# Kernel optimization log

Hardware: AMD Instinct MI355X
Metric: run time of the kernel (lower is better)

Reference implementation:

```python
import jax, jax.numpy as jnp
import numpy as np

B, S, DM = 2, 2048, 2048
H, KV, HD = 16, 4, 128
THETA = 10000.0
EPS = 1e-6


def _rmsnorm(x, scale):
    # flax nnx.RMSNorm with dtype=float32: x / sqrt(mean(x^2)+eps) * scale
    var = jnp.mean(jnp.square(x.astype(jnp.float32)), axis=-1, keepdims=True)
    return (x.astype(jnp.float32) * jax.lax.rsqrt(var + EPS)) * scale


def _apply_rope(x, positions, base):
    # x: [B, S, heads, HD]; positions: [1, S]
    half = HD // 2
    fraction = 2.0 * jnp.arange(half, dtype=jnp.float32) / HD
    timescale = base ** fraction                              # [HD/2]
    sinusoid = positions[..., None].astype(jnp.float32) / timescale  # [1, S, HD/2]
    sinusoid = sinusoid[..., None, :]                         # [1, S, 1, HD/2]
    sin, cos = jnp.sin(sinusoid), jnp.cos(sinusoid)
    x1, x2 = x[..., :half], x[..., half:]
    return jnp.concatenate([x1 * cos - x2 * sin, x2 * cos + x1 * sin], axis=-1).astype(x.dtype)


def setup_inputs() -> dict:
    key = jax.random.key(0)
    ks = jax.random.split(key, 7)
    w = lambda k, shape: jax.random.normal(k, shape, jnp.float32) * 0.02
    return {
        "x": jax.random.normal(ks[0], (B, S, DM), jnp.float32),
        "wq": w(ks[1], (DM, H, HD)),
        "wk": w(ks[2], (DM, KV, HD)),
        "wv": w(ks[3], (DM, KV, HD)),
        "wo": w(ks[4], (H, HD, DM)),
        "q_scale": jnp.ones((HD,), jnp.float32),
        "k_scale": jnp.ones((HD,), jnp.float32),
    }


def reference(x, wq, wk, wv, wo, q_scale, k_scale):
    # QKV projections (LinearGeneral hidden -> (heads, head_dim))
    q = jnp.einsum("bsd,dhk->bshk", x, wq)   # [B,S,H,HD]
    k = jnp.einsum("bsd,dhk->bshk", x, wk)   # [B,S,KV,HD]
    v = jnp.einsum("bsd,dhk->bshk", x, wv)   # [B,S,KV,HD]
    # qk RMSNorm + cast back to compute dtype
    q = _rmsnorm(q, q_scale).astype(x.dtype)
    k = _rmsnorm(k, k_scale).astype(x.dtype)
    # RoPE
    positions = jnp.arange(S)[None, :]
    q = _apply_rope(q, positions, THETA)
    k = _apply_rope(k, positions, THETA)
    # GQA attention: group query heads per kv head instead of materializing repeat_kv
    G = H // KV
    qg = q.reshape(B, S, KV, G, HD) * (HD ** -0.5)
    scores = jnp.einsum("bqkgd,bskd->bkgqs", qg, k)           # [B,KV,G,S,S]
    causal = jnp.tril(jnp.ones((S, S), jnp.bool_))
    scores = jnp.where(causal, scores, jnp.finfo(scores.dtype).min)
    probs = jax.nn.softmax(scores, axis=-1)
    att = jnp.einsum("bkgqs,bskd->bqkgd", probs, v).reshape(B, S, H, HD)
    # output projection contracting (heads, head_dim)
    return jnp.einsum("bshd,hdo->bso", att, wo)
```

## Files before the change

kernel.cpp:

```cpp
#include <hip/hip_runtime.h>
#include <hip/hip_bf16.h>
#include <math.h>

typedef unsigned short u16;
typedef short short8 __attribute__((ext_vector_type(8)));
typedef float floatx4 __attribute__((ext_vector_type(4)));

#define B_   2
#define S_   2048
#define DM_  2048
#define H_   16
#define KVH_ 4
#define HD_  128

__device__ __forceinline__ float bf2f(u16 v) {
  union { unsigned int u; float f; } x; x.u = ((unsigned int)v) << 16; return x.f;
}
__device__ __forceinline__ u16 f2bf(float f) {
  union { float f; unsigned int u; } x; x.f = f;
  unsigned int u = x.u;
  u += 0x7FFFu + ((u >> 16) & 1u);
  return (u16)(u >> 16);
}

#define GLDS16(gp, lp) __builtin_amdgcn_global_load_lds( \
    (const __attribute__((address_space(1))) unsigned int*)(const void*)(gp), \
    (__attribute__((address_space(3))) unsigned int*)(void*)(lp), 16, 0, 0)

__global__ __launch_bounds__(256) void k_prep(
    const float* __restrict__ x, const float* __restrict__ wq,
    const float* __restrict__ wk, const float* __restrict__ wv,
    const float* __restrict__ wo,
    u16* __restrict__ x_bf, u16* __restrict__ wqkv_t, u16* __restrict__ wo_t)
{
  int bx = blockIdx.x;
  if (bx < 8192) {
    int i = bx * 256 + threadIdx.x;
    const float4 v = ((const float4*)x)[i];
    u16 o[4] = { f2bf(v.x), f2bf(v.y), f2bf(v.z), f2bf(v.w) };
    *(unsigned long long*)(x_bf + (size_t)i * 4) = *(unsigned long long*)o;
    return;
  }
  bx -= 8192;
  const float* src; u16* dst; int C, cb;
  if (bx < 4096)      { src = wq; dst = wqkv_t; C = 2048; cb = 64; }
  else if (bx < 5120) { bx -= 4096; src = wk; dst = wqkv_t + (size_t)2048 * 2048; C = 512; cb = 16; }
  else if (bx < 6144) { bx -= 5120; src = wv; dst = wqkv_t + (size_t)2560 * 2048; C = 512; cb = 16; }
  else                { bx -= 6144; src = wo; dst = wo_t; C = 2048; cb = 64; }
  const int R = 2048;
  int c0 = (bx % cb) * 32, r0 = (bx / cb) * 32;
  __shared__ float tile[32][33];
  int tx = threadIdx.x & 31, ty = threadIdx.x >> 5;
#pragma unroll
  for (int j = 0; j < 4; j++)
    tile[ty * 4 + j][tx] = src[(size_t)(r0 + ty * 4 + j) * C + c0 + tx];
  __syncthreads();
#pragma unroll
  for (int j = 0; j < 4; j++)
    dst[(size_t)(c0 + ty * 4 + j) * R + r0 + tx] = f2bf(tile[tx][ty * 4 + j]);
}

__global__ __launch_bounds__(256, 3) void k_gemm_bt(
    const u16* __restrict__ A, const u16* __restrict__ Bt,
    void* __restrict__ Cout, int M, int N, int K, int c_bf16)
{
  __shared__ u16 As[128 * 64];
  __shared__ u16 Bs[128 * 64];
  int tid = threadIdx.x;
  int lane = tid & 63;
  int quad = lane >> 4, l16 = lane & 15;
  int wid = tid >> 6;
  int m0 = blockIdx.y * 128, n0 = blockIdx.x * 128;
  int wm = (wid >> 1) * 64, wn = (wid & 1) * 64;

  floatx4 acc[4][4] = {};

  int srow = tid >> 3;
  int gjc0 = (tid & 7) ^ (srow & 7);
  const u16* Ap = A + (size_t)(m0 + srow) * K + gjc0 * 8;
  const u16* Bp = Bt + (size_t)(n0 + srow) * K + gjc0 * 8;
  u16* AsW = As + tid * 8;
  u16* BsW = Bs + tid * 8;

  for (int kt = 0; kt < K; kt += 64) {
    __syncthreads();
#pragma unroll
    for (int j = 0; j < 4; j++) {
      GLDS16(Ap + (size_t)(j * 32) * K, AsW + j * 2048);
      GLDS16(Bp + (size_t)(j * 32) * K, BsW + j * 2048);
    }
    Ap += 64; Bp += 64;
    __syncthreads();

#pragma unroll
    for (int ks = 0; ks < 2; ks++) {
      short8 af[4], bfv[4];
#pragma unroll
      for (int mi = 0; mi < 4; mi++) {
        int row = wm + mi * 16 + l16;
        af[mi] = *(const short8*)&As[row * 64 + (((ks * 4 + quad) ^ (row & 7)) * 8)];
      }
#pragma unroll
      for (int ni = 0; ni < 4; ni++) {
        int row = wn + ni * 16 + l16;
        bfv[ni] = *(const short8*)&Bs[row * 64 + (((ks * 4 + quad) ^ (row & 7)) * 8)];
      }
#pragma unroll
      for (int mi = 0; mi < 4; mi++)
#pragma unroll
        for (int ni = 0; ni < 4; ni++)
          acc[mi][ni] = __builtin_amdgcn_mfma_f32_16x16x32_bf16(
              af[mi], bfv[ni], acc[mi][ni], 0, 0, 0);
    }
  }

#pragma unroll
  for (int mi = 0; mi < 4; mi++)
#pragma unroll
    for (int ni = 0; ni < 4; ni++)
#pragma unroll
      for (int r = 0; r < 4; r++) {
        int row = m0 + wm + mi * 16 + quad * 4 + r;
        int col = n0 + wn + ni * 16 + l16;
        float v = acc[mi][ni][r];
        if (c_bf16) ((u16*)Cout)[(size_t)row * N + col] = f2bf(v);
        else        ((float*)Cout)[(size_t)row * N + col] = v;
      }
}

__global__ __launch_bounds__(256) void k_post(
    const u16* __restrict__ C1, const float* __restrict__ qs,
    const float* __restrict__ ks, u16* __restrict__ qr, u16* __restrict__ kr,
    u16* __restrict__ vt)
{
  int bx = blockIdx.x;
  if (bx < 4096) {
    int m = bx;
    int lane = threadIdx.x & 63, wid = threadIdx.x >> 6;
    int pos = m & (S_ - 1);
    float ts = powf(10000.0f, (float)lane * (1.0f / 64.0f));
    float ang = (float)pos / ts;
    float sn = sinf(ang), cs = cosf(ang);
    for (int r = wid; r < H_ + KVH_; r += 4) {
      bool isq = r < H_;
      const u16* src = C1 + (size_t)m * 3072 + (isq ? r * HD_ : DM_ + (r - H_) * HD_);
      float x1 = bf2f(src[lane]), x2 = bf2f(src[lane + 64]);
      float ss = x1 * x1 + x2 * x2;
#pragma unroll
      for (int d = 1; d < 64; d <<= 1) ss += __shfl_xor(ss, d);
      float rs = rsqrtf(ss * (1.0f / 128.0f) + 1e-6f);
      const float* sc = isq ? qs : ks;
      float y1 = x1 * rs * sc[lane];
      float y2 = x2 * rs * sc[lane + 64];
      float o1 = y1 * cs - y2 * sn;
      float o2 = y2 * cs + y1 * sn;
      if (isq) { o1 *= 0.088388347648318447f; o2 *= 0.088388347648318447f; }
      u16* dst = isq ? (qr + ((size_t)m * H_ + r) * HD_)
                     : (kr + ((size_t)m * KVH_ + (r - H_)) * HD_);
      dst[lane]      = f2bf(o1);
      dst[lane + 64] = f2bf(o2);
    }
    return;
  }
  bx -= 4096;
  int sx = bx & 63, rest = bx >> 6;
  int hy = rest & 3, bk = rest >> 2;
  int s0 = sx * 32, h0 = hy * 32;
  int b = bk >> 2, kv = bk & 3;
  __shared__ u16 tile[32][33];
  int tx = threadIdx.x & 31, ty = threadIdx.x >> 5;
#pragma unroll
  for (int j = 0; j < 4; j++)
    tile[ty * 4 + j][tx] =
        C1[(size_t)(b * S_ + s0 + ty * 4 + j) * 3072 + 2560 + kv * HD_ + h0 + tx];
  __syncthreads();
#pragma unroll
  for (int j = 0; j < 4; j++)
    vt[((size_t)bk * HD_ + h0 + ty * 4 + j) * S_ + s0 + tx] = tile[tx][ty * 4 + j];
}

__global__ __launch_bounds__(256, 3) void k_flash(
    const u16* __restrict__ qr, const u16* __restrict__ kr,
    const u16* __restrict__ vt, u16* __restrict__ att)
{
  __shared__ u16 Ks[64 * 128];
  __shared__ u16 Vt[128 * 64];
  __shared__ u16 Ps[4][16 * 72];
  int tid = threadIdx.x, lane = tid & 63, wid = tid >> 6;
  int quad = lane >> 4, l16 = lane & 15;
  int bx = blockIdx.x;
  int it = 31 - (bx >> 5);
  int hb = bx & 31;
  int h = hb & 15, b = hb >> 4;
  int kvh = h >> 2;
  int q0 = it * 64;

  short8 qf[4];
  {
    const u16* qb = qr + ((size_t)(b * S_ + q0 + wid * 16 + l16) * H_ + h) * HD_;
#pragma unroll
    for (int kk = 0; kk < 4; kk++)
      qf[kk] = *(const short8*)(qb + kk * 32 + quad * 8);
  }

  int gjk = (tid & 15) ^ ((tid >> 4) & 15);
  int gjv = (tid & 7) ^ ((tid >> 3) & 7);
  const u16* kp = kr + ((size_t)(b * S_ + (tid >> 4)) * KVH_ + kvh) * HD_ + gjk * 8;
  const u16* vp = vt + ((size_t)(b * KVH_ + kvh) * HD_ + (tid >> 3)) * S_ + gjv * 8;

  short8 pk[4], pv[4];
#pragma unroll
  for (int j = 0; j < 4; j++) {
    pk[j] = *(const short8*)(kp + (size_t)j * 16 * KVH_ * HD_);
    pv[j] = *(const short8*)(vp + (size_t)j * 32 * S_);
  }

  floatx4 accO[8] = {};
  float lp[4] = { 0.f, 0.f, 0.f, 0.f };
  u16* PsW = &Ps[wid][0];
  int qrow_hi = q0 + wid * 16 + quad * 4;

  const float LOG2E = 1.4426950408889634f;
  const float MBIAS = -12.5f * 1.4426950408889634f;

  for (int kt = 0; kt <= it; kt++) {
    int k0 = kt * 64;
#pragma unroll
    for (int j = 0; j < 4; j++) {
      *(short8*)&Ks[(j * 256 + tid) * 8] = pk[j];
      *(short8*)&Vt[(j * 256 + tid) * 8] = pv[j];
    }
    __syncthreads();

    if (kt < it) {
      kp += (size_t)64 * KVH_ * HD_;
      vp += 64;
#pragma unroll
      for (int j = 0; j < 4; j++) {
        pk[j] = *(const short8*)(kp + (size_t)j * 16 * KVH_ * HD_);
        pv[j] = *(const short8*)(vp + (size_t)j * 32 * S_);
      }
    }

    floatx4 sacc[4] = {};
#pragma unroll
    for (int kk = 0; kk < 4; kk++)
#pragma unroll
      for (int nt = 0; nt < 4; nt++) {
        int row = nt * 16 + l16;
        short8 kf = *(const short8*)&Ks[row * 128 + (((kk * 4 + quad) ^ (row & 15)) * 8)];
        sacc[nt] = __builtin_amdgcn_mfma_f32_16x16x32_bf16(qf[kk], kf, sacc[nt], 0, 0, 0);
      }

    bool diag = (kt == it);
#pragma unroll
    for (int r = 0; r < 4; r++) {
      int row = qrow_hi + r;
      float rsum = 0.f;
#pragma unroll
      for (int nt = 0; nt < 4; nt++) {
        float p = __builtin_amdgcn_exp2f(fmaf(sacc[nt][r], LOG2E, MBIAS));
        if (diag && (k0 + nt * 16 + l16) > row) p = 0.f;
        rsum += p;
        PsW[(quad * 4 + r) * 72 + nt * 16 + l16] = f2bf(p);
      }
      lp[r] += rsum;
    }

#pragma unroll
    for (int kk = 0; kk < 2; kk++) {
      short8 pf = *(const short8*)&PsW[l16 * 72 + kk * 32 + quad * 8];
#pragma unroll
      for (int ht = 0; ht < 8; ht++) {
        int row = ht * 16 + l16;
        short8 vf = *(const short8*)&Vt[row * 64 + (((kk * 4 + quad) ^ (row & 7)) * 8)];
        accO[ht] = __builtin_amdgcn_mfma_f32_16x16x32_bf16(pf, vf, accO[ht], 0, 0, 0);
      }
    }
    __syncthreads();
  }

#pragma unroll
  for (int r = 0; r < 4; r++) {
#pragma unroll
    for (int d = 1; d < 16; d <<= 1) lp[r] += __shfl_xor(lp[r], d);
    lp[r] = 1.0f / lp[r];
  }

#pragma unroll
  for (int ht = 0; ht < 8; ht++)
#pragma unroll
    for (int r = 0; r < 4; r++) {
      int row = qrow_hi + r;
      att[((size_t)(b * S_ + row) * H_ + h) * HD_ + ht * 16 + l16] = f2bf(accO[ht][r] * lp[r]);
    }
}

extern "C" void kernel_launch(void* const* d_in, const int* in_sizes, int n_in,
                              void* d_out, int out_size, void* d_ws, size_t ws_size,
                              hipStream_t stream)
{
  const float* x  = (const float*)d_in[0];
  const float* wq = (const float*)d_in[1];
  const float* wk = (const float*)d_in[2];
  const float* wv = (const float*)d_in[3];
  const float* wo = (const float*)d_in[4];
  const float* qs = (const float*)d_in[5];
  const float* ks = (const float*)d_in[6];

  char* ws = (char*)d_ws;
  size_t off = 0;
  u16* x_bf   = (u16*)(ws + off); off += (size_t)4096 * 2048 * 2;
  u16* wqkv_t = (u16*)(ws + off); off += (size_t)3072 * 2048 * 2;
  u16* wo_t   = (u16*)(ws + off); off += (size_t)2048 * 2048 * 2;
  u16* C1     = (u16*)(ws + off); off += (size_t)4096 * 3072 * 2;
  u16* q_rope = (u16*)(ws + off); off += (size_t)4096 * 16 * 128 * 2;
  u16* k_rope = (u16*)(ws + off); off += (size_t)4096 * 4 * 128 * 2;
  u16* vt     = (u16*)(ws + off); off += (size_t)8 * 128 * 2048 * 2;
  u16* att    = (u16*)(ws + off); off += (size_t)4096 * 2048 * 2;

  k_prep<<<dim3(18432), 256, 0, stream>>>(x, wq, wk, wv, wo, x_bf, wqkv_t, wo_t);

  k_gemm_bt<<<dim3(24, 32), 256, 0, stream>>>(x_bf, wqkv_t, C1, 4096, 3072, 2048, 1);

  k_post<<<dim3(6144), 256, 0, stream>>>(C1, qs, ks, q_rope, k_rope, vt);

  k_flash<<<dim3(1024), 256, 0, stream>>>(q_rope, k_rope, vt, att);

  k_gemm_bt<<<dim3(16, 32), 256, 0, stream>>>(att, wo_t, d_out, 4096, 2048, 2048, 0);

  (void)in_sizes; (void)n_in; (void)out_size; (void)ws_size;
}
```

Measured before the change: 297.6 us.

## Restructure flash attention to 2 waves each owning 32 query rows

The flash attention kernel now runs 128 threads (2 waves) per block instead of 256 (4 waves). Each wave handles two 16-row query tiles, so every K and V fragment read from LDS feeds two MFMAs. The P buffer gets an XOR-swizzled layout, and s_setprio is raised around the MFMA sections. The intent is to cut LDS traffic per MFMA and raise compute density. The cost is higher register pressure, more global loads per thread for staging, and fewer waves per block to hide latency.

```diff
diff --git a/kernel.cpp b/kernel.cpp
--- a/kernel.cpp
+++ b/kernel.cpp
@@ -179,13 +179,13 @@
     vt[((size_t)bk * HD_ + h0 + ty * 4 + j) * S_ + s0 + tx] = tile[tx][ty * 4 + j];
 }
 
-__global__ __launch_bounds__(256, 3) void k_flash(
+__global__ __launch_bounds__(128, 2) void k_flash(
     const u16* __restrict__ qr, const u16* __restrict__ kr,
     const u16* __restrict__ vt, u16* __restrict__ att)
 {
   __shared__ u16 Ks[64 * 128];
   __shared__ u16 Vt[128 * 64];
-  __shared__ u16 Ps[4][16 * 72];
+  __shared__ u16 Ps[2][32 * 64];
   int tid = threadIdx.x, lane = tid & 63, wid = tid >> 6;
   int quad = lane >> 4, l16 = lane & 15;
   int bx = blockIdx.x;
@@ -195,30 +195,30 @@
   int kvh = h >> 2;
   int q0 = it * 64;
 
-  short8 qf[4];
-  {
-    const u16* qb = qr + ((size_t)(b * S_ + q0 + wid * 16 + l16) * H_ + h) * HD_;
+  short8 qf[2][4];
+#pragma unroll
+  for (int m = 0; m < 2; m++) {
+    const u16* qb = qr + ((size_t)(b * S_ + q0 + wid * 32 + m * 16 + l16) * H_ + h) * HD_;
 #pragma unroll
     for (int kk = 0; kk < 4; kk++)
-      qf[kk] = *(const short8*)(qb + kk * 32 + quad * 8);
-  }
-
-  int gjk = (tid & 15) ^ ((tid >> 4) & 15);
-  int gjv = (tid & 7) ^ ((tid >> 3) & 7);
-  const u16* kp = kr + ((size_t)(b * S_ + (tid >> 4)) * KVH_ + kvh) * HD_ + gjk * 8;
-  const u16* vp = vt + ((size_t)(b * KVH_ + kvh) * HD_ + (tid >> 3)) * S_ + gjv * 8;
-
-  short8 pk[4], pv[4];
-#pragma unroll
-  for (int j = 0; j < 4; j++) {
-    pk[j] = *(const short8*)(kp + (size_t)j * 16 * KVH_ * HD_);
-    pv[j] = *(const short8*)(vp + (size_t)j * 32 * S_);
-  }
-
-  floatx4 accO[8] = {};
-  float lp[4] = { 0.f, 0.f, 0.f, 0.f };
+      qf[m][kk] = *(const short8*)(qb + kk * 32 + quad * 8);
+  }
+
+  int gK = (tid & 15) ^ (tid >> 4);
+  int gV = (tid & 7) ^ ((tid >> 3) & 7);
+  const u16* kp = kr + ((size_t)(b * S_ + (tid >> 4)) * KVH_ + kvh) * HD_;
+  const u16* vp = vt + ((size_t)(b * KVH_ + kvh) * HD_ + (tid >> 3)) * S_ + gV * 8;
+
+  short8 pk[8], pv[8];
+#pragma unroll
+  for (int j = 0; j < 8; j++) {
+    pk[j] = *(const short8*)(kp + (size_t)(j * 8) * KVH_ * HD_ + (gK ^ ((j & 1) << 3)) * 8);
+    pv[j] = *(const short8*)(vp + (size_t)(j * 16) * S_);
+  }
+
+  floatx4 accO[2][8] = {};
+  float lp[2][4] = {};
   u16* PsW = &Ps[wid][0];
-  int qrow_hi = q0 + wid * 16 + quad * 4;
 
   const float LOG2E = 1.4426950408889634f;
   const float MBIAS = -12.5f * 1.4426950408889634f;
@@ -226,9 +226,9 @@
   for (int kt = 0; kt <= it; kt++) {
     int k0 = kt * 64;
 #pragma unroll
-    for (int j = 0; j < 4; j++) {
-      *(short8*)&Ks[(j * 256 + tid) * 8] = pk[j];
-      *(short8*)&Vt[(j * 256 + tid) * 8] = pv[j];
+    for (int j = 0; j < 8; j++) {
+      *(short8*)&Ks[(j * 128 + tid) * 8] = pk[j];
+      *(short8*)&Vt[(j * 128 + tid) * 8] = pv[j];
     }
     __syncthreads();
 
@@ -236,64 +236,88 @@
       kp += (size_t)64 * KVH_ * HD_;
       vp += 64;
 #pragma unroll
-      for (int j = 0; j < 4; j++) {
-        pk[j] = *(const short8*)(kp + (size_t)j * 16 * KVH_ * HD_);
-        pv[j] = *(const short8*)(vp + (size_t)j * 32 * S_);
-      }
-    }
-
-    floatx4 sacc[4] = {};
-#pragma unroll
-    for (int kk = 0; kk < 4; kk++)
+      for (int j = 0; j < 8; j++) {
+        pk[j] = *(const short8*)(kp + (size_t)(j * 8) * KVH_ * HD_ + (gK ^ ((j & 1) << 3)) * 8);
+        pv[j] = *(const short8*)(vp + (size_t)(j * 16) * S_);
+      }
+    }
+
+    floatx4 sacc[2][4] = {};
+    __builtin_amdgcn_s_setprio(1);
+#pragma unroll
+    for (int kk = 0; kk < 4; kk++) {
+      short8 kf[4];
 #pragma unroll
       for (int nt = 0; nt < 4; nt++) {
         int row = nt * 16 + l16;
-        short8 kf = *(const short8*)&Ks[row * 128 + (((kk * 4 + quad) ^ (row & 15)) * 8)];
-        sacc[nt] = __builtin_amdgcn_mfma_f32_16x16x32_bf16(qf[kk], kf, sacc[nt], 0, 0, 0);
-      }
+        kf[nt] = *(const short8*)&Ks[row * 128 + (((kk * 4 + quad) ^ (row & 15)) * 8)];
+      }
+#pragma unroll
+      for (int nt = 0; nt < 4; nt++) {
+        sacc[0][nt] = __builtin_amdgcn_mfma_f32_16x16x32_bf16(qf[0][kk], kf[nt], sacc[0][nt], 0, 0, 0);
+        sacc[1][nt] = __builtin_amdgcn_mfma_f32_16x16x32_bf16(qf[1][kk], kf[nt], sacc[1][nt], 0, 0, 0);
+      }
+    }
+    __builtin_amdgcn_s_setprio(0);
 
     bool diag = (kt == it);
 #pragma unroll
-    for (int r = 0; r < 4; r++) {
-      int row = qrow_hi + r;
-      float rsum = 0.f;
-#pragma unroll
-      for (int nt = 0; nt < 4; nt++) {
-        float p = __builtin_amdgcn_exp2f(fmaf(sacc[nt][r], LOG2E, MBIAS));
-        if (diag && (k0 + nt * 16 + l16) > row) p = 0.f;
-        rsum += p;
-        PsW[(quad * 4 + r) * 72 + nt * 16 + l16] = f2bf(p);
-      }
-      lp[r] += rsum;
-    }
-
+    for (int m = 0; m < 2; m++)
+#pragma unroll
+      for (int r = 0; r < 4; r++) {
+        int prow = m * 16 + quad * 4 + r;
+        int qrow = q0 + wid * 32 + prow;
+        float rsum = 0.f;
+#pragma unroll
+        for (int nt = 0; nt < 4; nt++) {
+          float p = __builtin_amdgcn_exp2f(fmaf(sacc[m][nt][r], LOG2E, MBIAS));
+          if (diag && (k0 + nt * 16 + l16) > qrow) p = 0.f;
+          rsum += p;
+          PsW[prow * 64 + (((nt * 2 + (l16 >> 3)) ^ (prow & 7)) * 8) + (l16 & 7)] = f2bf(p);
+        }
+        lp[m][r] += rsum;
+      }
+
+    __builtin_amdgcn_s_setprio(1);
 #pragma unroll
     for (int kk = 0; kk < 2; kk++) {
-      short8 pf = *(const short8*)&PsW[l16 * 72 + kk * 32 + quad * 8];
+      short8 pf[2];
+#pragma unroll
+      for (int m = 0; m < 2; m++) {
+        int prow = m * 16 + l16;
+        pf[m] = *(const short8*)&PsW[prow * 64 + (((kk * 4 + quad) ^ (prow & 7)) * 8)];
+      }
 #pragma unroll
       for (int ht = 0; ht < 8; ht++) {
         int row = ht * 16 + l16;
         short8 vf = *(const short8*)&Vt[row * 64 + (((kk * 4 + quad) ^ (row & 7)) * 8)];
-        accO[ht] = __builtin_amdgcn_mfma_f32_16x16x32_bf16(pf, vf, accO[ht], 0, 0, 0);
-      }
-    }
+        accO[0][ht] = __builtin_amdgcn_mfma_f32_16x16x32_bf16(pf[0], vf, accO[0][ht], 0, 0, 0);
+        accO[1][ht] = __builtin_amdgcn_mfma_f32_16x16x32_bf16(pf[1], vf, accO[1][ht], 0, 0, 0);
+      }
+    }
+    __builtin_amdgcn_s_setprio(0);
     __syncthreads();
   }
 
 #pragma unroll
-  for (int r = 0; r < 4; r++) {
-#pragma unroll
-    for (int d = 1; d < 16; d <<= 1) lp[r] += __shfl_xor(lp[r], d);
-    lp[r] = 1.0f / lp[r];
-  }
-
-#pragma unroll
-  for (int ht = 0; ht < 8; ht++)
+  for (int m = 0; m < 2; m++)
 #pragma unroll
     for (int r = 0; r < 4; r++) {
-      int row = qrow_hi + r;
-      att[((size_t)(b * S_ + row) * H_ + h) * HD_ + ht * 16 + l16] = f2bf(accO[ht][r] * lp[r]);
-    }
+#pragma unroll
+      for (int d = 1; d < 16; d <<= 1) lp[m][r] += __shfl_xor(lp[m][r], d);
+      lp[m][r] = 1.0f / lp[m][r];
+    }
+
+#pragma unroll
+  for (int m = 0; m < 2; m++)
+#pragma unroll
+    for (int ht = 0; ht < 8; ht++)
+#pragma unroll
+      for (int r = 0; r < 4; r++) {
+        int row = q0 + wid * 32 + m * 16 + quad * 4 + r;
+        att[((size_t)(b * S_ + row) * H_ + h) * HD_ + ht * 16 + l16] =
+            f2bf(accO[m][ht][r] * lp[m][r]);
+      }
 }
 
 extern "C" void kernel_launch(void* const* d_in, const int* in_sizes, int n_in,
@@ -325,7 +349,7 @@
 
   k_post<<<dim3(6144), 256, 0, stream>>>(C1, qs, ks, q_rope, k_rope, vt);
 
-  k_flash<<<dim3(1024), 256, 0, stream>>>(q_rope, k_rope, vt, att);
+  k_flash<<<dim3(1024), 128, 0, stream>>>(q_rope, k_rope, vt, att);
 
   k_gemm_bt<<<dim3(16, 32), 256, 0, stream>>>(att, wo_t, d_out, 4096, 2048, 2048, 0);
 
```

New measurement: 336.5 us. +13.0%, slower.
